# Optimization experiments

Hardware: AMD Instinct MI355X
Metric: run time of the kernel (lower is better)

## Reference

```python
import jax, jax.numpy as jnp
import numpy as np

N_NODES = 10000
N_EDGES = 320000
D_IN = 256
D_OUT = 256
MAX_NORM = 0.95

def setup_inputs() -> dict:
    key = jax.random.key(0)
    ks = jax.random.split(key, 7)
    x = jax.random.normal(ks[0], (N_NODES, D_IN), dtype=jnp.float32)
    edge_index = jax.random.randint(ks[1], (2, N_EDGES), 0, N_NODES, dtype=jnp.int64)
    # xavier-ish scales
    W = jax.random.normal(ks[2], (D_OUT, D_IN), dtype=jnp.float32) * (1.0 / np.sqrt(D_IN))
    b = jax.random.normal(ks[3], (D_OUT,), dtype=jnp.float32) * 0.02
    mag_w = jax.random.normal(ks[4], (1, D_IN), dtype=jnp.float32) * 0.02
    mag_b = jax.random.normal(ks[5], (1,), dtype=jnp.float32) * 0.02
    attn_w = jax.random.normal(ks[6], (1, 2 * D_OUT), dtype=jnp.float32) * (1.0 / np.sqrt(2 * D_OUT))
    return {"x": x, "edge_index": edge_index, "W": W, "b": b,
            "mag_w": mag_w, "mag_b": mag_b, "attn_w": attn_w}

def _expmap0(u):
    # Poincare ball exp map at origin, curvature c = 1.0
    un = jnp.linalg.norm(u, axis=-1, keepdims=True)
    un_c = jnp.maximum(un, 1e-15)
    return jnp.tanh(un_c) * u / un_c

def reference(x, edge_index, W, b, mag_w, mag_b, attn_w):
    N = x.shape[0]
    F_out = W.shape[0]
    # linear transform + directional/magnitude decomposition
    h_raw = x @ W.T + b                                              # (N, F)
    h_dir = h_raw / jnp.maximum(jnp.linalg.norm(h_raw, axis=-1, keepdims=True), 1e-12)
    h_mag = jax.nn.sigmoid(x @ mag_w.T + mag_b) * 1.5                # (N, 1)
    h = h_dir * h_mag                                                # (N, F)
    src, tgt = edge_index[0], edge_index[1]
    h_src = h[src]                                                   # (E, F)
    h_tgt = h[tgt]                                                   # (E, F)
    # attn(cat([h_src, h_tgt])) == h_src @ a_s + h_tgt @ a_t (avoids concat)
    a_s, a_t = attn_w[0, :F_out], attn_w[0, F_out:]
    scores = h_src @ a_s + h_tgt @ a_t                               # (E,)
    # scatter softmax over edges grouped by target node
    mx = jnp.maximum(jax.ops.segment_max(scores, tgt, num_segments=N), -1e9)
    ex = jnp.exp(scores - mx[tgt])
    se = jax.ops.segment_sum(ex, tgt, num_segments=N)
    attn_weights = ex / (se[tgt] + 1e-10)                            # (E,)
    # weighted message aggregation
    agg = jax.ops.segment_sum(h_src * attn_weights[:, None], tgt, num_segments=N)
    h_combined = h + agg
    h_poincare = _expmap0(h_combined)
    norms = jnp.linalg.norm(h_poincare, axis=1, keepdims=True)
    return jnp.where(norms > MAX_NORM, h_poincare * (MAX_NORM / (norms + 1e-8)), h_poincare)
```

## Files before the change

### kernel.cpp

```cpp
#include <hip/hip_runtime.h>
#include <math.h>

#define N_NODES 10000
#define N_EDGES 320000
#define D 256
#define CAP 128
#define BM 32
#define LDK 40
#define GB_GEMM ((N_NODES + BM - 1) / BM)
#define GB_BUILD ((N_EDGES + 255) / 256)

typedef __attribute__((ext_vector_type(8))) short short8;
typedef __attribute__((ext_vector_type(4))) float f32x4;

__device__ __forceinline__ ushort f2bf(float f) {
    union { float f; unsigned u; } v; v.f = f;
    unsigned r = v.u + 0x7FFFu + ((v.u >> 16) & 1u);
    return (ushort)(r >> 16);
}
__device__ __forceinline__ float bf2f(ushort u) {
    union { unsigned u; float f; } v; v.u = (unsigned)u << 16;
    return v.f;
}

__global__ __launch_bounds__(256) void k_prep(const float* __restrict__ W,
                                              ushort* __restrict__ Wb,
                                              unsigned* __restrict__ deg) {
    const int tid = blockIdx.x * 256 + threadIdx.x;
    const int i = tid * 4;
    const float4 v = *(const float4*)&W[i];
    ushort4 o;
    o.x = f2bf(v.x); o.y = f2bf(v.y); o.z = f2bf(v.z); o.w = f2bf(v.w);
    *(ushort4*)&Wb[i] = o;
    if (tid < N_NODES) deg[tid] = 0u;
}

__global__ __launch_bounds__(256) void k_main(const float* __restrict__ x,
                                              const ushort* __restrict__ Wb,
                                              const float* __restrict__ b,
                                              const float* __restrict__ mag_w,
                                              const float* __restrict__ mag_b,
                                              const float* __restrict__ attn_w,
                                              const int* __restrict__ ei,
                                              unsigned* __restrict__ deg,
                                              int* __restrict__ csr_src,
                                              ushort* __restrict__ hb,
                                              float* __restrict__ es) {
    if (blockIdx.x >= GB_GEMM) {
        const int e = (blockIdx.x - GB_GEMM) * 256 + threadIdx.x;
        if (e < N_EDGES) {
            int src = ei[e];
            int tgt = ei[N_EDGES + e];
            src = min(max(src, 0), N_NODES - 1);
            tgt = min(max(tgt, 0), N_NODES - 1);
            const unsigned slot = atomicAdd(&deg[tgt], 1u);
            if (slot < CAP) csr_src[(size_t)tgt * CAP + slot] = src;
        }
        return;
    }

    __shared__ ushort ldsA[BM * LDK];
    __shared__ ushort ldsB[256 * LDK];
    __shared__ float red_ssq[4][BM], red_ra[4][BM];
    __shared__ float smrow[BM], scl[BM];

    const int t = threadIdx.x;
    const int w = t >> 6, l = t & 63;
    const int bm = blockIdx.x * BM;
    const int sra = t >> 3, ka = (t & 7) * 4;
    const int am = bm + sra;
    const int srb = t >> 2, kb = (t & 3) * 8;

    const int fl = l & 15;
    const int fh = (l >> 4) * 8;

    f32x4 acc[2][4];
#pragma unroll
    for (int r = 0; r < 2; ++r)
#pragma unroll
        for (int c = 0; c < 4; ++c) acc[r][c] = (f32x4)(0.f);

    float sm_part = 0.f;

    for (int k0 = 0; k0 < D; k0 += 32) {
        float4 xa = make_float4(0.f, 0.f, 0.f, 0.f);
        if (am < N_NODES) xa = *(const float4*)&x[(size_t)am * D + k0 + ka];
        const float4 mwv = *(const float4*)&mag_w[k0 + ka];
        sm_part += xa.x * mwv.x + xa.y * mwv.y + xa.z * mwv.z + xa.w * mwv.w;
        short8 bv[4];
#pragma unroll
        for (int p = 0; p < 4; ++p)
            bv[p] = *(const short8*)&Wb[(size_t)(p * 64 + srb) * D + k0 + kb];
        __syncthreads();
        ushort4 av;
        av.x = f2bf(xa.x); av.y = f2bf(xa.y); av.z = f2bf(xa.z); av.w = f2bf(xa.w);
        *(ushort4*)&ldsA[sra * LDK + ka] = av;
#pragma unroll
        for (int p = 0; p < 4; ++p)
            *(short8*)&ldsB[(p * 64 + srb) * LDK + kb] = bv[p];
        __syncthreads();
        short8 af[2], bfr[4];
#pragma unroll
        for (int r = 0; r < 2; ++r)
            af[r] = *(short8*)&ldsA[(r * 16 + fl) * LDK + fh];
#pragma unroll
        for (int c = 0; c < 4; ++c)
            bfr[c] = *(short8*)&ldsB[(w * 64 + c * 16 + fl) * LDK + fh];
#pragma unroll
        for (int r = 0; r < 2; ++r)
#pragma unroll
            for (int c = 0; c < 4; ++c)
                acc[r][c] = __builtin_amdgcn_mfma_f32_16x16x32_bf16(af[r], bfr[c], acc[r][c], 0, 0, 0);
    }

#pragma unroll
    for (int o = 1; o < 8; o <<= 1) sm_part += __shfl_xor(sm_part, o);
    if ((t & 7) == 0) smrow[sra] = sm_part;

    float bn[4], asn[4];
#pragma unroll
    for (int c = 0; c < 4; ++c) {
        const int n = w * 64 + c * 16 + fl;
        bn[c]  = b[n];
        asn[c] = attn_w[n];
    }
    const int rq = (l >> 4) * 4;

#pragma unroll
    for (int r = 0; r < 2; ++r) {
#pragma unroll
        for (int reg = 0; reg < 4; ++reg) {
            float vssq = 0.f, vra = 0.f;
#pragma unroll
            for (int c = 0; c < 4; ++c) {
                const float v = acc[r][c][reg] + bn[c];
                vssq += v * v;
                vra  += v * asn[c];
            }
#pragma unroll
            for (int o = 1; o < 16; o <<= 1) {
                vssq += __shfl_xor(vssq, o);
                vra  += __shfl_xor(vra, o);
            }
            if (fl == 0) {
                const int m = r * 16 + rq + reg;
                red_ssq[w][m] = vssq;
                red_ra[w][m]  = vra;
            }
        }
    }
    __syncthreads();

    if (t < BM) {
        const int gm = bm + t;
        const float ssq = red_ssq[0][t] + red_ssq[1][t] + red_ssq[2][t] + red_ssq[3][t];
        const float ra  = red_ra[0][t]  + red_ra[1][t]  + red_ra[2][t]  + red_ra[3][t];
        const float norm = sqrtf(ssq);
        const float mag  = 1.5f / (1.f + expf(-(smrow[t] + mag_b[0])));
        const float scale = mag / fmaxf(norm, 1e-12f);
        scl[t] = scale;
        if (gm < N_NODES) es[gm] = expf(ra * scale);
    }
    __syncthreads();

#pragma unroll
    for (int r = 0; r < 2; ++r) {
#pragma unroll
        for (int reg = 0; reg < 4; ++reg) {
            const int ml = r * 16 + rq + reg;
            const int m = bm + ml;
            if (m < N_NODES) {
                const float scale = scl[ml];
#pragma unroll
                for (int c = 0; c < 4; ++c) {
                    const int n = w * 64 + c * 16 + fl;
                    hb[(size_t)m * D + n] = f2bf((acc[r][c][reg] + bn[c]) * scale);
                }
            }
        }
    }
}

__global__ __launch_bounds__(256) void k_agg(const ushort* __restrict__ hb,
                                             const unsigned* __restrict__ deg,
                                             const int* __restrict__ csr_src,
                                             const float* __restrict__ es,
                                             float* __restrict__ out) {
    const int wv = threadIdx.x >> 6;
    const int n = blockIdx.x * 4 + wv;
    const int lane = threadIdx.x & 63;
    const int d = min((int)deg[n], CAP);
    const size_t cbase = (size_t)n * CAP;

    int src0 = 0, src1 = 0;
    float w0 = 0.f, w1 = 0.f;
    if (lane < d)      { src0 = csr_src[cbase + lane];      w0 = es[src0]; }
    if (lane + 64 < d) { src1 = csr_src[cbase + lane + 64]; w1 = es[src1]; }
    float sum = w0 + w1;
#pragma unroll
    for (int o = 32; o > 0; o >>= 1) sum += __shfl_xor(sum, o);
    const float inv = 1.f / (sum + 1e-10f);

    const int coff = lane * 4;
    float4 A0 = make_float4(0.f, 0.f, 0.f, 0.f), A1 = A0, A2 = A0, A3 = A0;

    {
        const int cnt = min(d, 64);
        int e = 0;
        for (; e + 4 <= cnt; e += 4) {
            const int s0 = __shfl(src0, e), s1 = __shfl(src0, e + 1);
            const int s2 = __shfl(src0, e + 2), s3 = __shfl(src0, e + 3);
            const float q0 = __shfl(w0, e),     q1 = __shfl(w0, e + 1);
            const float q2 = __shfl(w0, e + 2), q3 = __shfl(w0, e + 3);
            const ushort4 v0 = *(const ushort4*)&hb[(size_t)s0 * D + coff];
            const ushort4 v1 = *(const ushort4*)&hb[(size_t)s1 * D + coff];
            const ushort4 v2 = *(const ushort4*)&hb[(size_t)s2 * D + coff];
            const ushort4 v3 = *(const ushort4*)&hb[(size_t)s3 * D + coff];
            A0.x += q0 * bf2f(v0.x); A0.y += q0 * bf2f(v0.y); A0.z += q0 * bf2f(v0.z); A0.w += q0 * bf2f(v0.w);
            A1.x += q1 * bf2f(v1.x); A1.y += q1 * bf2f(v1.y); A1.z += q1 * bf2f(v1.z); A1.w += q1 * bf2f(v1.w);
            A2.x += q2 * bf2f(v2.x); A2.y += q2 * bf2f(v2.y); A2.z += q2 * bf2f(v2.z); A2.w += q2 * bf2f(v2.w);
            A3.x += q3 * bf2f(v3.x); A3.y += q3 * bf2f(v3.y); A3.z += q3 * bf2f(v3.z); A3.w += q3 * bf2f(v3.w);
        }
        for (; e < cnt; ++e) {
            const int s0 = __shfl(src0, e);
            const float q0 = __shfl(w0, e);
            const ushort4 v0 = *(const ushort4*)&hb[(size_t)s0 * D + coff];
            A0.x += q0 * bf2f(v0.x); A0.y += q0 * bf2f(v0.y); A0.z += q0 * bf2f(v0.z); A0.w += q0 * bf2f(v0.w);
        }
    }
    if (d > 64) {
        const int cnt = d - 64;
        int e = 0;
        for (; e + 4 <= cnt; e += 4) {
            const int s0 = __shfl(src1, e), s1 = __shfl(src1, e + 1);
            const int s2 = __shfl(src1, e + 2), s3 = __shfl(src1, e + 3);
            const float q0 = __shfl(w1, e),     q1 = __shfl(w1, e + 1);
            const float q2 = __shfl(w1, e + 2), q3 = __shfl(w1, e + 3);
            const ushort4 v0 = *(const ushort4*)&hb[(size_t)s0 * D + coff];
            const ushort4 v1 = *(const ushort4*)&hb[(size_t)s1 * D + coff];
            const ushort4 v2 = *(const ushort4*)&hb[(size_t)s2 * D + coff];
            const ushort4 v3 = *(const ushort4*)&hb[(size_t)s3 * D + coff];
            A0.x += q0 * bf2f(v0.x); A0.y += q0 * bf2f(v0.y); A0.z += q0 * bf2f(v0.z); A0.w += q0 * bf2f(v0.w);
            A1.x += q1 * bf2f(v1.x); A1.y += q1 * bf2f(v1.y); A1.z += q1 * bf2f(v1.z); A1.w += q1 * bf2f(v1.w);
            A2.x += q2 * bf2f(v2.x); A2.y += q2 * bf2f(v2.y); A2.z += q2 * bf2f(v2.z); A2.w += q2 * bf2f(v2.w);
            A3.x += q3 * bf2f(v3.x); A3.y += q3 * bf2f(v3.y); A3.z += q3 * bf2f(v3.z); A3.w += q3 * bf2f(v3.w);
        }
        for (; e < cnt; ++e) {
            const int s0 = __shfl(src1, e);
            const float q0 = __shfl(w1, e);
            const ushort4 v0 = *(const ushort4*)&hb[(size_t)s0 * D + coff];
            A0.x += q0 * bf2f(v0.x); A0.y += q0 * bf2f(v0.y); A0.z += q0 * bf2f(v0.z); A0.w += q0 * bf2f(v0.w);
        }
    }
    float4 acc = make_float4((A0.x + A1.x + A2.x + A3.x) * inv,
                             (A0.y + A1.y + A2.y + A3.y) * inv,
                             (A0.z + A1.z + A2.z + A3.z) * inv,
                             (A0.w + A1.w + A2.w + A3.w) * inv);

    const ushort4 hnv = *(const ushort4*)&hb[(size_t)n * D + coff];
    float4 u = make_float4(bf2f(hnv.x) + acc.x, bf2f(hnv.y) + acc.y,
                           bf2f(hnv.z) + acc.z, bf2f(hnv.w) + acc.w);
    float ssq = u.x * u.x + u.y * u.y + u.z * u.z + u.w * u.w;
#pragma unroll
    for (int o = 32; o > 0; o >>= 1) ssq += __shfl_xor(ssq, o);
    const float un = sqrtf(ssq);
    const float un_c = fmaxf(un, 1e-15f);
    const float th = tanhf(un_c);
    float s = th / un_c;
    const float pn = th * (un / un_c);
    if (pn > 0.95f) s *= 0.95f / (pn + 1e-8f);
    float4 p = make_float4(u.x * s, u.y * s, u.z * s, u.w * s);
    *(float4*)&out[(size_t)n * D + coff] = p;
}

extern "C" void kernel_launch(void* const* d_in, const int* in_sizes, int n_in,
                              void* d_out, int out_size, void* d_ws, size_t ws_size,
                              hipStream_t stream) {
    const float* x      = (const float*)d_in[0];
    const int*   ei     = (const int*)d_in[1];
    const float* W      = (const float*)d_in[2];
    const float* b      = (const float*)d_in[3];
    const float* mag_w  = (const float*)d_in[4];
    const float* mag_b  = (const float*)d_in[5];
    const float* attn_w = (const float*)d_in[6];
    float* out = (float*)d_out;

    char* ws = (char*)d_ws;
    ushort* hb = (ushort*)ws;         ws += (size_t)N_NODES * D * sizeof(ushort);
    float* es = (float*)ws;           ws += (size_t)N_NODES * sizeof(float);
    unsigned* deg = (unsigned*)ws;    ws += (size_t)N_NODES * sizeof(unsigned);
    int* csr_src = (int*)ws;          ws += (size_t)N_NODES * CAP * sizeof(int);
    ushort* Wb = (ushort*)ws;         ws += (size_t)D * D * sizeof(ushort);

    k_prep<<<(D * D) / (256 * 4), 256, 0, stream>>>(W, Wb, deg);
    k_main<<<GB_GEMM + GB_BUILD, 256, 0, stream>>>(
        x, Wb, b, mag_w, mag_b, attn_w, ei, deg, csr_src, hb, es);
    k_agg<<<N_NODES / 4, 256, 0, stream>>>(hb, deg, csr_src, es, out);
}
```

Before: 57.83 us.

## Fuse prep, GEMM/CSR-build and aggregation into one cooperative persistent kernel

Replaces the three kernel launches with a single cooperative kernel that loops over jobs in grid-stride fashion and separates the phases with grid-wide syncs. It is meant to remove launch overhead and the gaps between kernels. In exchange, grid size is capped at 1024 blocks (occupancy times 256 CUs), so every block must walk through many jobs. Grid syncs add their own cost, and the launch bounds hint may change register allocation.

```diff
diff --git a/kernel.cpp b/kernel.cpp
--- a/kernel.cpp
+++ b/kernel.cpp
@@ -1,5 +1,8 @@
 #include <hip/hip_runtime.h>
+#include <hip/hip_cooperative_groups.h>
 #include <math.h>
+
+namespace cg = cooperative_groups;
 
 #define N_NODES 10000
 #define N_EDGES 320000
@@ -9,6 +12,7 @@
 #define LDK 40
 #define GB_GEMM ((N_NODES + BM - 1) / BM)
 #define GB_BUILD ((N_EDGES + 255) / 256)
+#define N_AGG (N_NODES / 4)
 
 typedef __attribute__((ext_vector_type(8))) short short8;
 typedef __attribute__((ext_vector_type(4))) float f32x4;
@@ -23,254 +27,259 @@
     return v.f;
 }
 
-__global__ __launch_bounds__(256) void k_prep(const float* __restrict__ W,
-                                              ushort* __restrict__ Wb,
-                                              unsigned* __restrict__ deg) {
-    const int tid = blockIdx.x * 256 + threadIdx.x;
-    const int i = tid * 4;
-    const float4 v = *(const float4*)&W[i];
-    ushort4 o;
-    o.x = f2bf(v.x); o.y = f2bf(v.y); o.z = f2bf(v.z); o.w = f2bf(v.w);
-    *(ushort4*)&Wb[i] = o;
-    if (tid < N_NODES) deg[tid] = 0u;
-}
-
-__global__ __launch_bounds__(256) void k_main(const float* __restrict__ x,
-                                              const ushort* __restrict__ Wb,
-                                              const float* __restrict__ b,
-                                              const float* __restrict__ mag_w,
-                                              const float* __restrict__ mag_b,
-                                              const float* __restrict__ attn_w,
-                                              const int* __restrict__ ei,
-                                              unsigned* __restrict__ deg,
-                                              int* __restrict__ csr_src,
-                                              ushort* __restrict__ hb,
-                                              float* __restrict__ es) {
-    if (blockIdx.x >= GB_GEMM) {
-        const int e = (blockIdx.x - GB_GEMM) * 256 + threadIdx.x;
-        if (e < N_EDGES) {
-            int src = ei[e];
-            int tgt = ei[N_EDGES + e];
-            src = min(max(src, 0), N_NODES - 1);
-            tgt = min(max(tgt, 0), N_NODES - 1);
-            const unsigned slot = atomicAdd(&deg[tgt], 1u);
-            if (slot < CAP) csr_src[(size_t)tgt * CAP + slot] = src;
-        }
-        return;
+__global__ __launch_bounds__(256, 4) void k_all(const float* __restrict__ x,
+                                                const int* __restrict__ ei,
+                                                const float* __restrict__ W,
+                                                const float* __restrict__ b,
+                                                const float* __restrict__ mag_w,
+                                                const float* __restrict__ mag_b,
+                                                const float* __restrict__ attn_w,
+                                                unsigned* __restrict__ deg,
+                                                int* __restrict__ csr_src,
+                                                ushort* __restrict__ hb,
+                                                float* __restrict__ es,
+                                                ushort* __restrict__ Wb,
+                                                float* __restrict__ out) {
+    cg::grid_group grid = cg::this_grid();
+    const int t = threadIdx.x;
+    const int nthread = gridDim.x * 256;
+
+    for (int tid = blockIdx.x * 256 + t; tid < (D * D) / 4; tid += nthread) {
+        const float4 v = *(const float4*)&W[tid * 4];
+        ushort4 o;
+        o.x = f2bf(v.x); o.y = f2bf(v.y); o.z = f2bf(v.z); o.w = f2bf(v.w);
+        *(ushort4*)&Wb[tid * 4] = o;
     }
-
-    __shared__ ushort ldsA[BM * LDK];
-    __shared__ ushort ldsB[256 * LDK];
-    __shared__ float red_ssq[4][BM], red_ra[4][BM];
-    __shared__ float smrow[BM], scl[BM];
-
-    const int t = threadIdx.x;
-    const int w = t >> 6, l = t & 63;
-    const int bm = blockIdx.x * BM;
-    const int sra = t >> 3, ka = (t & 7) * 4;
-    const int am = bm + sra;
-    const int srb = t >> 2, kb = (t & 3) * 8;
-
-    const int fl = l & 15;
-    const int fh = (l >> 4) * 8;
-
-    f32x4 acc[2][4];
-#pragma unroll
-    for (int r = 0; r < 2; ++r)
-#pragma unroll
-        for (int c = 0; c < 4; ++c) acc[r][c] = (f32x4)(0.f);
-
-    float sm_part = 0.f;
-
-    for (int k0 = 0; k0 < D; k0 += 32) {
-        float4 xa = make_float4(0.f, 0.f, 0.f, 0.f);
-        if (am < N_NODES) xa = *(const float4*)&x[(size_t)am * D + k0 + ka];
-        const float4 mwv = *(const float4*)&mag_w[k0 + ka];
-        sm_part += xa.x * mwv.x + xa.y * mwv.y + xa.z * mwv.z + xa.w * mwv.w;
-        short8 bv[4];
-#pragma unroll
-        for (int p = 0; p < 4; ++p)
-            bv[p] = *(const short8*)&Wb[(size_t)(p * 64 + srb) * D + k0 + kb];
-        __syncthreads();
-        ushort4 av;
-        av.x = f2bf(xa.x); av.y = f2bf(xa.y); av.z = f2bf(xa.z); av.w = f2bf(xa.w);
-        *(ushort4*)&ldsA[sra * LDK + ka] = av;
-#pragma unroll
-        for (int p = 0; p < 4; ++p)
-            *(short8*)&ldsB[(p * 64 + srb) * LDK + kb] = bv[p];
-        __syncthreads();
-        short8 af[2], bfr[4];
-#pragma unroll
-        for (int r = 0; r < 2; ++r)
-            af[r] = *(short8*)&ldsA[(r * 16 + fl) * LDK + fh];
-#pragma unroll
-        for (int c = 0; c < 4; ++c)
-            bfr[c] = *(short8*)&ldsB[(w * 64 + c * 16 + fl) * LDK + fh];
-#pragma unroll
-        for (int r = 0; r < 2; ++r)
-#pragma unroll
-            for (int c = 0; c < 4; ++c)
-                acc[r][c] = __builtin_amdgcn_mfma_f32_16x16x32_bf16(af[r], bfr[c], acc[r][c], 0, 0, 0);
-    }
-
-#pragma unroll
-    for (int o = 1; o < 8; o <<= 1) sm_part += __shfl_xor(sm_part, o);
-    if ((t & 7) == 0) smrow[sra] = sm_part;
-
-    float bn[4], asn[4];
-#pragma unroll
-    for (int c = 0; c < 4; ++c) {
-        const int n = w * 64 + c * 16 + fl;
-        bn[c]  = b[n];
-        asn[c] = attn_w[n];
-    }
-    const int rq = (l >> 4) * 4;
-
-#pragma unroll
-    for (int r = 0; r < 2; ++r) {
-#pragma unroll
-        for (int reg = 0; reg < 4; ++reg) {
-            float vssq = 0.f, vra = 0.f;
+    for (int tid = blockIdx.x * 256 + t; tid < N_NODES; tid += nthread)
+        deg[tid] = 0u;
+    grid.sync();
+
+    {
+        __shared__ ushort ldsA[BM * LDK];
+        __shared__ ushort ldsB[256 * LDK];
+        __shared__ float red_ssq[4][BM], red_ra[4][BM];
+        __shared__ float smrow[BM], scl[BM];
+
+        const int w = t >> 6, l = t & 63;
+        const int sra = t >> 3, ka = (t & 7) * 4;
+        const int srb = t >> 2, kb = (t & 3) * 8;
+        const int fl = l & 15;
+        const int fh = (l >> 4) * 8;
+        const int rq = (l >> 4) * 4;
+
+        for (int job = blockIdx.x; job < GB_GEMM + GB_BUILD; job += gridDim.x) {
+            if (job >= GB_GEMM) {
+                const int e = (job - GB_GEMM) * 256 + t;
+                if (e < N_EDGES) {
+                    int src = ei[e];
+                    int tgt = ei[N_EDGES + e];
+                    src = min(max(src, 0), N_NODES - 1);
+                    tgt = min(max(tgt, 0), N_NODES - 1);
+                    const unsigned slot = atomicAdd(&deg[tgt], 1u);
+                    if (slot < CAP) csr_src[(size_t)tgt * CAP + slot] = src;
+                }
+                continue;
+            }
+            const int bm = job * BM;
+            const int am = bm + sra;
+
+            f32x4 acc[2][4];
+#pragma unroll
+            for (int r = 0; r < 2; ++r)
+#pragma unroll
+                for (int c = 0; c < 4; ++c) acc[r][c] = (f32x4)(0.f);
+            float sm_part = 0.f;
+
+            for (int k0 = 0; k0 < D; k0 += 32) {
+                float4 xa = make_float4(0.f, 0.f, 0.f, 0.f);
+                if (am < N_NODES) xa = *(const float4*)&x[(size_t)am * D + k0 + ka];
+                const float4 mwv = *(const float4*)&mag_w[k0 + ka];
+                sm_part += xa.x * mwv.x + xa.y * mwv.y + xa.z * mwv.z + xa.w * mwv.w;
+                short8 bv[4];
+#pragma unroll
+                for (int p = 0; p < 4; ++p)
+                    bv[p] = *(const short8*)&Wb[(size_t)(p * 64 + srb) * D + k0 + kb];
+                __syncthreads();
+                ushort4 av;
+                av.x = f2bf(xa.x); av.y = f2bf(xa.y); av.z = f2bf(xa.z); av.w = f2bf(xa.w);
+                *(ushort4*)&ldsA[sra * LDK + ka] = av;
+#pragma unroll
+                for (int p = 0; p < 4; ++p)
+                    *(short8*)&ldsB[(p * 64 + srb) * LDK + kb] = bv[p];
+                __syncthreads();
+                short8 af[2], bfr[4];
+#pragma unroll
+                for (int r = 0; r < 2; ++r)
+                    af[r] = *(short8*)&ldsA[(r * 16 + fl) * LDK + fh];
+#pragma unroll
+                for (int c = 0; c < 4; ++c)
+                    bfr[c] = *(short8*)&ldsB[(w * 64 + c * 16 + fl) * LDK + fh];
+#pragma unroll
+                for (int r = 0; r < 2; ++r)
+#pragma unroll
+                    for (int c = 0; c < 4; ++c)
+                        acc[r][c] = __builtin_amdgcn_mfma_f32_16x16x32_bf16(af[r], bfr[c], acc[r][c], 0, 0, 0);
+            }
+
+            float smp = sm_part;
+#pragma unroll
+            for (int o = 1; o < 8; o <<= 1) smp += __shfl_xor(smp, o);
+            if ((t & 7) == 0) smrow[sra] = smp;
+
+            float bn[4], asn[4];
 #pragma unroll
             for (int c = 0; c < 4; ++c) {
-                const float v = acc[r][c][reg] + bn[c];
-                vssq += v * v;
-                vra  += v * asn[c];
-            }
-#pragma unroll
-            for (int o = 1; o < 16; o <<= 1) {
-                vssq += __shfl_xor(vssq, o);
-                vra  += __shfl_xor(vra, o);
-            }
-            if (fl == 0) {
-                const int m = r * 16 + rq + reg;
-                red_ssq[w][m] = vssq;
-                red_ra[w][m]  = vra;
+                const int n = w * 64 + c * 16 + fl;
+                bn[c]  = b[n];
+                asn[c] = attn_w[n];
+            }
+
+#pragma unroll
+            for (int r = 0; r < 2; ++r) {
+#pragma unroll
+                for (int reg = 0; reg < 4; ++reg) {
+                    float vssq = 0.f, vra = 0.f;
+#pragma unroll
+                    for (int c = 0; c < 4; ++c) {
+                        const float v = acc[r][c][reg] + bn[c];
+                        vssq += v * v;
+                        vra  += v * asn[c];
+                    }
+#pragma unroll
+                    for (int o = 1; o < 16; o <<= 1) {
+                        vssq += __shfl_xor(vssq, o);
+                        vra  += __shfl_xor(vra, o);
+                    }
+                    if (fl == 0) {
+                        const int m = r * 16 + rq + reg;
+                        red_ssq[w][m] = vssq;
+                        red_ra[w][m]  = vra;
+                    }
+                }
+            }
+            __syncthreads();
+
+            if (t < BM) {
+                const int gm = bm + t;
+                const float ssq = red_ssq[0][t] + red_ssq[1][t] + red_ssq[2][t] + red_ssq[3][t];
+                const float ra  = red_ra[0][t]  + red_ra[1][t]  + red_ra[2][t]  + red_ra[3][t];
+                const float norm = sqrtf(ssq);
+                const float mag  = 1.5f / (1.f + expf(-(smrow[t] + mag_b[0])));
+                const float scale = mag / fmaxf(norm, 1e-12f);
+                scl[t] = scale;
+                if (gm < N_NODES) es[gm] = expf(ra * scale);
+            }
+            __syncthreads();
+
+#pragma unroll
+            for (int r = 0; r < 2; ++r) {
+#pragma unroll
+                for (int reg = 0; reg < 4; ++reg) {
+                    const int ml = r * 16 + rq + reg;
+                    const int m = bm + ml;
+                    if (m < N_NODES) {
+                        const float scale = scl[ml];
+#pragma unroll
+                        for (int c = 0; c < 4; ++c) {
+                            const int n = w * 64 + c * 16 + fl;
+                            hb[(size_t)m * D + n] = f2bf((acc[r][c][reg] + bn[c]) * scale);
+                        }
+                    }
+                }
             }
         }
     }
-    __syncthreads();
-
-    if (t < BM) {
-        const int gm = bm + t;
-        const float ssq = red_ssq[0][t] + red_ssq[1][t] + red_ssq[2][t] + red_ssq[3][t];
-        const float ra  = red_ra[0][t]  + red_ra[1][t]  + red_ra[2][t]  + red_ra[3][t];
-        const float norm = sqrtf(ssq);
-        const float mag  = 1.5f / (1.f + expf(-(smrow[t] + mag_b[0])));
-        const float scale = mag / fmaxf(norm, 1e-12f);
-        scl[t] = scale;
-        if (gm < N_NODES) es[gm] = expf(ra * scale);
-    }
-    __syncthreads();
-
-#pragma unroll
-    for (int r = 0; r < 2; ++r) {
-#pragma unroll
-        for (int reg = 0; reg < 4; ++reg) {
-            const int ml = r * 16 + rq + reg;
-            const int m = bm + ml;
-            if (m < N_NODES) {
-                const float scale = scl[ml];
-#pragma unroll
-                for (int c = 0; c < 4; ++c) {
-                    const int n = w * 64 + c * 16 + fl;
-                    hb[(size_t)m * D + n] = f2bf((acc[r][c][reg] + bn[c]) * scale);
-                }
-            }
+    grid.sync();
+
+    {
+        const int wv = threadIdx.x >> 6;
+        const int lane = threadIdx.x & 63;
+        const int coff = lane * 4;
+
+        for (int jb = blockIdx.x; jb < N_AGG; jb += gridDim.x) {
+            const int n = jb * 4 + wv;
+            const int d = min((int)deg[n], CAP);
+            const size_t cbase = (size_t)n * CAP;
+
+            int src0 = 0, src1 = 0;
+            float w0 = 0.f, w1 = 0.f;
+            if (lane < d)      { src0 = csr_src[cbase + lane];      w0 = es[src0]; }
+            if (lane + 64 < d) { src1 = csr_src[cbase + lane + 64]; w1 = es[src1]; }
+            float sum = w0 + w1;
+#pragma unroll
+            for (int o = 32; o > 0; o >>= 1) sum += __shfl_xor(sum, o);
+            const float inv = 1.f / (sum + 1e-10f);
+
+            float4 A0 = make_float4(0.f, 0.f, 0.f, 0.f), A1 = A0, A2 = A0, A3 = A0;
+            {
+                const int cnt = min(d, 64);
+                int e = 0;
+                for (; e + 4 <= cnt; e += 4) {
+                    const int s0 = __shfl(src0, e), s1 = __shfl(src0, e + 1);
+                    const int s2 = __shfl(src0, e + 2), s3 = __shfl(src0, e + 3);
+                    const float q0 = __shfl(w0, e),     q1 = __shfl(w0, e + 1);
+                    const float q2 = __shfl(w0, e + 2), q3 = __shfl(w0, e + 3);
+                    const ushort4 v0 = *(const ushort4*)&hb[(size_t)s0 * D + coff];
+                    const ushort4 v1 = *(const ushort4*)&hb[(size_t)s1 * D + coff];
+                    const ushort4 v2 = *(const ushort4*)&hb[(size_t)s2 * D + coff];
+                    const ushort4 v3 = *(const ushort4*)&hb[(size_t)s3 * D + coff];
+                    A0.x += q0 * bf2f(v0.x); A0.y += q0 * bf2f(v0.y); A0.z += q0 * bf2f(v0.z); A0.w += q0 * bf2f(v0.w);
+                    A1.x += q1 * bf2f(v1.x); A1.y += q1 * bf2f(v1.y); A1.z += q1 * bf2f(v1.z); A1.w += q1 * bf2f(v1.w);
+                    A2.x += q2 * bf2f(v2.x); A2.y += q2 * bf2f(v2.y); A2.z += q2 * bf2f(v2.z); A2.w += q2 * bf2f(v2.w);
+                    A3.x += q3 * bf2f(v3.x); A3.y += q3 * bf2f(v3.y); A3.z += q3 * bf2f(v3.z); A3.w += q3 * bf2f(v3.w);
+                }
+                for (; e < cnt; ++e) {
+                    const int s0 = __shfl(src0, e);
+                    const float q0 = __shfl(w0, e);
+                    const ushort4 v0 = *(const ushort4*)&hb[(size_t)s0 * D + coff];
+                    A0.x += q0 * bf2f(v0.x); A0.y += q0 * bf2f(v0.y); A0.z += q0 * bf2f(v0.z); A0.w += q0 * bf2f(v0.w);
+                }
+            }
+            if (d > 64) {
+                const int cnt = d - 64;
+                int e = 0;
+                for (; e + 4 <= cnt; e += 4) {
+                    const int s0 = __shfl(src1, e), s1 = __shfl(src1, e + 1);
+                    const int s2 = __shfl(src1, e + 2), s3 = __shfl(src1, e + 3);
+                    const float q0 = __shfl(w1, e),     q1 = __shfl(w1, e + 1);
+                    const float q2 = __shfl(w1, e + 2), q3 = __shfl(w1, e + 3);
+                    const ushort4 v0 = *(const ushort4*)&hb[(size_t)s0 * D + coff];
+                    const ushort4 v1 = *(const ushort4*)&hb[(size_t)s1 * D + coff];
+                    const ushort4 v2 = *(const ushort4*)&hb[(size_t)s2 * D + coff];
+                    const ushort4 v3 = *(const ushort4*)&hb[(size_t)s3 * D + coff];
+                    A0.x += q0 * bf2f(v0.x); A0.y += q0 * bf2f(v0.y); A0.z += q0 * bf2f(v0.z); A0.w += q0 * bf2f(v0.w);
+                    A1.x += q1 * bf2f(v1.x); A1.y += q1 * bf2f(v1.y); A1.z += q1 * bf2f(v1.z); A1.w += q1 * bf2f(v1.w);
+                    A2.x += q2 * bf2f(v2.x); A2.y += q2 * bf2f(v2.y); A2.z += q2 * bf2f(v2.z); A2.w += q2 * bf2f(v2.w);
+                    A3.x += q3 * bf2f(v3.x); A3.y += q3 * bf2f(v3.y); A3.z += q3 * bf2f(v3.z); A3.w += q3 * bf2f(v3.w);
+                }
+                for (; e < cnt; ++e) {
+                    const int s0 = __shfl(src1, e);
+                    const float q0 = __shfl(w1, e);
+                    const ushort4 v0 = *(const ushort4*)&hb[(size_t)s0 * D + coff];
+                    A0.x += q0 * bf2f(v0.x); A0.y += q0 * bf2f(v0.y); A0.z += q0 * bf2f(v0.z); A0.w += q0 * bf2f(v0.w);
+                }
+            }
+            float4 acc4 = make_float4((A0.x + A1.x + A2.x + A3.x) * inv,
+                                      (A0.y + A1.y + A2.y + A3.y) * inv,
+                                      (A0.z + A1.z + A2.z + A3.z) * inv,
+                                      (A0.w + A1.w + A2.w + A3.w) * inv);
+
+            const ushort4 hnv = *(const ushort4*)&hb[(size_t)n * D + coff];
+            float4 u = make_float4(bf2f(hnv.x) + acc4.x, bf2f(hnv.y) + acc4.y,
+                                   bf2f(hnv.z) + acc4.z, bf2f(hnv.w) + acc4.w);
+            float ssq = u.x * u.x + u.y * u.y + u.z * u.z + u.w * u.w;
+#pragma unroll
+            for (int o = 32; o > 0; o >>= 1) ssq += __shfl_xor(ssq, o);
+            const float un = sqrtf(ssq);
+            const float un_c = fmaxf(un, 1e-15f);
+            const float th = tanhf(un_c);
+            float s = th / un_c;
+            const float pn = th * (un / un_c);
+            if (pn > 0.95f) s *= 0.95f / (pn + 1e-8f);
+            float4 p = make_float4(u.x * s, u.y * s, u.z * s, u.w * s);
+            *(float4*)&out[(size_t)n * D + coff] = p;
         }
     }
-}
-
-__global__ __launch_bounds__(256) void k_agg(const ushort* __restrict__ hb,
-                                             const unsigned* __restrict__ deg,
-                                             const int* __restrict__ csr_src,
-                                             const float* __restrict__ es,
-                                             float* __restrict__ out) {
-    const int wv = threadIdx.x >> 6;
-    const int n = blockIdx.x * 4 + wv;
-    const int lane = threadIdx.x & 63;
-    const int d = min((int)deg[n], CAP);
-    const size_t cbase = (size_t)n * CAP;
-
-    int src0 = 0, src1 = 0;
-    float w0 = 0.f, w1 = 0.f;
-    if (lane < d)      { src0 = csr_src[cbase + lane];      w0 = es[src0]; }
-    if (lane + 64 < d) { src1 = csr_src[cbase + lane + 64]; w1 = es[src1]; }
-    float sum = w0 + w1;
-#pragma unroll
-    for (int o = 32; o > 0; o >>= 1) sum += __shfl_xor(sum, o);
-    const float inv = 1.f / (sum + 1e-10f);
-
-    const int coff = lane * 4;
-    float4 A0 = make_float4(0.f, 0.f, 0.f, 0.f), A1 = A0, A2 = A0, A3 = A0;
-
-    {
-        const int cnt = min(d, 64);
-        int e = 0;
-        for (; e + 4 <= cnt; e += 4) {
-            const int s0 = __shfl(src0, e), s1 = __shfl(src0, e + 1);
-            const int s2 = __shfl(src0, e + 2), s3 = __shfl(src0, e + 3);
-            const float q0 = __shfl(w0, e),     q1 = __shfl(w0, e + 1);
-            const float q2 = __shfl(w0, e + 2), q3 = __shfl(w0, e + 3);
-            const ushort4 v0 = *(const ushort4*)&hb[(size_t)s0 * D + coff];
-            const ushort4 v1 = *(const ushort4*)&hb[(size_t)s1 * D + coff];
-            const ushort4 v2 = *(const ushort4*)&hb[(size_t)s2 * D + coff];
-            const ushort4 v3 = *(const ushort4*)&hb[(size_t)s3 * D + coff];
-            A0.x += q0 * bf2f(v0.x); A0.y += q0 * bf2f(v0.y); A0.z += q0 * bf2f(v0.z); A0.w += q0 * bf2f(v0.w);
-            A1.x += q1 * bf2f(v1.x); A1.y += q1 * bf2f(v1.y); A1.z += q1 * bf2f(v1.z); A1.w += q1 * bf2f(v1.w);
-            A2.x += q2 * bf2f(v2.x); A2.y += q2 * bf2f(v2.y); A2.z += q2 * bf2f(v2.z); A2.w += q2 * bf2f(v2.w);
-            A3.x += q3 * bf2f(v3.x); A3.y += q3 * bf2f(v3.y); A3.z += q3 * bf2f(v3.z); A3.w += q3 * bf2f(v3.w);
-        }
-        for (; e < cnt; ++e) {
-            const int s0 = __shfl(src0, e);
-            const float q0 = __shfl(w0, e);
-            const ushort4 v0 = *(const ushort4*)&hb[(size_t)s0 * D + coff];
-            A0.x += q0 * bf2f(v0.x); A0.y += q0 * bf2f(v0.y); A0.z += q0 * bf2f(v0.z); A0.w += q0 * bf2f(v0.w);
-        }
-    }
-    if (d > 64) {
-        const int cnt = d - 64;
-        int e = 0;
-        for (; e + 4 <= cnt; e += 4) {
-            const int s0 = __shfl(src1, e), s1 = __shfl(src1, e + 1);
-            const int s2 = __shfl(src1, e + 2), s3 = __shfl(src1, e + 3);
-            const float q0 = __shfl(w1, e),     q1 = __shfl(w1, e + 1);
-            const float q2 = __shfl(w1, e + 2), q3 = __shfl(w1, e + 3);
-            const ushort4 v0 = *(const ushort4*)&hb[(size_t)s0 * D + coff];
-            const ushort4 v1 = *(const ushort4*)&hb[(size_t)s1 * D + coff];
-            const ushort4 v2 = *(const ushort4*)&hb[(size_t)s2 * D + coff];
-            const ushort4 v3 = *(const ushort4*)&hb[(size_t)s3 * D + coff];
-            A0.x += q0 * bf2f(v0.x); A0.y += q0 * bf2f(v0.y); A0.z += q0 * bf2f(v0.z); A0.w += q0 * bf2f(v0.w);
-            A1.x += q1 * bf2f(v1.x); A1.y += q1 * bf2f(v1.y); A1.z += q1 * bf2f(v1.z); A1.w += q1 * bf2f(v1.w);
-            A2.x += q2 * bf2f(v2.x); A2.y += q2 * bf2f(v2.y); A2.z += q2 * bf2f(v2.z); A2.w += q2 * bf2f(v2.w);
-            A3.x += q3 * bf2f(v3.x); A3.y += q3 * bf2f(v3.y); A3.z += q3 * bf2f(v3.z); A3.w += q3 * bf2f(v3.w);
-        }
-        for (; e < cnt; ++e) {
-            const int s0 = __shfl(src1, e);
-            const float q0 = __shfl(w1, e);
-            const ushort4 v0 = *(const ushort4*)&hb[(size_t)s0 * D + coff];
-            A0.x += q0 * bf2f(v0.x); A0.y += q0 * bf2f(v0.y); A0.z += q0 * bf2f(v0.z); A0.w += q0 * bf2f(v0.w);
-        }
-    }
-    float4 acc = make_float4((A0.x + A1.x + A2.x + A3.x) * inv,
-                             (A0.y + A1.y + A2.y + A3.y) * inv,
-                             (A0.z + A1.z + A2.z + A3.z) * inv,
-                             (A0.w + A1.w + A2.w + A3.w) * inv);
-
-    const ushort4 hnv = *(const ushort4*)&hb[(size_t)n * D + coff];
-    float4 u = make_float4(bf2f(hnv.x) + acc.x, bf2f(hnv.y) + acc.y,
-                           bf2f(hnv.z) + acc.z, bf2f(hnv.w) + acc.w);
-    float ssq = u.x * u.x + u.y * u.y + u.z * u.z + u.w * u.w;
-#pragma unroll
-    for (int o = 32; o > 0; o >>= 1) ssq += __shfl_xor(ssq, o);
-    const float un = sqrtf(ssq);
-    const float un_c = fmaxf(un, 1e-15f);
-    const float th = tanhf(un_c);
-    float s = th / un_c;
-    const float pn = th * (un / un_c);
-    if (pn > 0.95f) s *= 0.95f / (pn + 1e-8f);
-    float4 p = make_float4(u.x * s, u.y * s, u.z * s, u.w * s);
-    *(float4*)&out[(size_t)n * D + coff] = p;
 }
 
 extern "C" void kernel_launch(void* const* d_in, const int* in_sizes, int n_in,
@@ -292,8 +301,15 @@
     int* csr_src = (int*)ws;          ws += (size_t)N_NODES * CAP * sizeof(int);
     ushort* Wb = (ushort*)ws;         ws += (size_t)D * D * sizeof(ushort);
 
-    k_prep<<<(D * D) / (256 * 4), 256, 0, stream>>>(W, Wb, deg);
-    k_main<<<GB_GEMM + GB_BUILD, 256, 0, stream>>>(
-        x, Wb, b, mag_w, mag_b, attn_w, ei, deg, csr_src, hb, es);
-    k_agg<<<N_NODES / 4, 256, 0, stream>>>(hb, deg, csr_src, es, out);
+    int nb = 0;
+    hipOccupancyMaxActiveBlocksPerMultiprocessor(&nb, k_all, 256, 0);
+    if (nb < 1) nb = 1;
+    long long grid = (long long)nb * 256;
+    if (grid > 1024) grid = 1024;
+
+    void* args[] = {(void*)&x, (void*)&ei, (void*)&W, (void*)&b, (void*)&mag_w,
+                    (void*)&mag_b, (void*)&attn_w, (void*)&deg, (void*)&csr_src,
+                    (void*)&hb, (void*)&es, (void*)&Wb, (void*)&out};
+    hipLaunchCooperativeKernel((const void*)k_all, dim3((int)grid), dim3(256),
+                               args, 0, stream);
 }
```

Result: slower. 185.7 us (+221.1%).
